# Optimization experiments

Measured on AMD Instinct MI355X. Metric: run time of the kernel, lower is better.

Reference implementation:

```python
import jax, jax.numpy as jnp
import numpy as np

NUM_CAT = 16
SEG_LENS = np.array([4, 2, 2, 4, 4, 3, 3, 2, 4, 6, 2, 6, 3, 3, 3, 3], dtype=np.int64)
SHIFTS = np.concatenate([[0], np.cumsum(SEG_LENS)[:-1]]).astype(np.int64)
MAX_SEG_COUNT = int(SEG_LENS.max())           # 6
MAX_SEG = int(SHIFTS[-1] + SEG_LENS[-1] - 1)  # 53
IN = 128
N = 65536
EPS = 1e-5  # BatchNorm1d default eps
SLOPE = 0.2  # LeakyReLU negative slope


def setup_inputs() -> dict:
    key = jax.random.key(0)
    ks = jax.random.split(key, 4)
    features = jax.random.normal(ks[0], (N, IN), dtype=jnp.float32)
    category_labels = jax.random.randint(ks[1], (N,), 0, NUM_CAT, dtype=jnp.int64)
    # channel raising MLP: Linear(IN -> NUM_CAT*IN, bias=False)
    W1 = jax.random.normal(ks[2], (IN, NUM_CAT * IN), dtype=jnp.float32) * (1.0 / np.sqrt(IN))
    gamma = jnp.ones((NUM_CAT * IN,), dtype=jnp.float32)
    beta = jnp.zeros((NUM_CAT * IN,), dtype=jnp.float32)
    # UnaryConv weight: xavier_normal over (NUM_CAT, IN, MAX_SEG_COUNT)
    W2 = jax.random.normal(ks[3], (NUM_CAT, IN, MAX_SEG_COUNT), dtype=jnp.float32) * np.sqrt(2.0 / (IN + MAX_SEG_COUNT))
    bias = jnp.zeros((MAX_SEG_COUNT,), dtype=jnp.float32)
    return dict(features=features, W1=W1, gamma=gamma, beta=beta, W2=W2, bias=bias,
                category_labels=category_labels)


def reference(features, W1, gamma, beta, W2, bias, category_labels):
    n = features.shape[0]
    # channel raising: Linear -> BatchNorm1d (batch stats) -> LeakyReLU(0.2)
    h = features @ W1                                   # [N, C*D]
    mean = h.mean(axis=0)
    var = h.var(axis=0)                                 # biased, as in torch BN
    h = (h - mean) / jnp.sqrt(var + EPS) * gamma + beta
    h = jnp.where(h >= 0, h, SLOPE * h)
    # per-category batched matmul classifier
    h = h.reshape(n, NUM_CAT, IN).transpose(1, 0, 2)    # [C, N, D]
    logits_all = jnp.einsum('cnd,cds->cns', h, W2) + bias  # [C, N, S]
    n_idx = jnp.arange(n)
    logits = logits_all[category_labels, n_idx]         # gather: [N, S]
    logsm = jax.nn.log_softmax(logits, axis=-1)
    # scatter into per-category segment ranges of the [N, MAX_SEG+1] output
    shifts = jnp.asarray(SHIFTS)[category_labels]       # [N]
    seg_len = jnp.asarray(SEG_LENS)[category_labels]    # [N]
    s_idx = jnp.arange(MAX_SEG_COUNT)
    valid = s_idx[None, :] < seg_len[:, None]           # [N, S]
    cols = jnp.clip(shifts[:, None] + s_idx[None, :], 0, MAX_SEG)
    vals = jnp.where(valid, logsm, 0.0)                 # invalid slots add 0
    out = jnp.zeros((n, MAX_SEG + 1), dtype=logsm.dtype)
    out = out.at[n_idx[:, None], cols].add(vals)
    return out
```

## Files before the change

kernel.cpp:

```cpp
#include <hip/hip_runtime.h>
#include <hip/hip_bf16.h>

#define NCAT 16

typedef __attribute__((ext_vector_type(8))) short short8v;
typedef __attribute__((ext_vector_type(4))) float float4v;
typedef __attribute__((ext_vector_type(16))) float f32x16;

__constant__ int c_shift[NCAT] = {0,4,6,8,12,16,19,22,24,28,34,36,42,45,48,51};
__constant__ int c_len[NCAT]   = {4,2,2,4,4,3,3,2,4,6,2,6,3,3,3,3};


static inline __device__ unsigned pk2(float lo, float hi) {
  float2 f2; f2.x = lo; f2.y = hi;
  __hip_bfloat162 h = __float22bfloat162_rn(f2);
  unsigned u; __builtin_memcpy(&u, &h, 4);
  return u;
}
static inline __device__ float bf2f(unsigned short v) {
  unsigned u = (unsigned)v << 16;
  float f; __builtin_memcpy(&f, &u, 4);
  return f;
}

template<bool PART>
__global__ __launch_bounds__(1024) void k_stats_m(
    const float* __restrict__ F, const float* __restrict__ W1,
    const float* __restrict__ W2,
    float* __restrict__ Gdst, unsigned* __restrict__ Gp16,
    float* __restrict__ sv, float* __restrict__ svpart,
    unsigned short* __restrict__ Wlb, float* __restrict__ W2p)
{
  const int tid = threadIdx.x;
  if (blockIdx.x >= 256) {
    const int cat = (int)blockIdx.x - 256;
    for (int e = tid; e < 2048; e += 1024) {
      const int fid = e >> 6, l = e & 63;
      const int ks = fid >> 3, ct = fid & 7;
      const int kb = 32 * ks + 8 * (l >> 4);
      const int c = cat * 128 + 16 * ct + (l & 15);
      uint4 pk;
      pk.x = pk2(W1[(size_t)(kb + 0) * 2048 + c], W1[(size_t)(kb + 1) * 2048 + c]);
      pk.y = pk2(W1[(size_t)(kb + 2) * 2048 + c], W1[(size_t)(kb + 3) * 2048 + c]);
      pk.z = pk2(W1[(size_t)(kb + 4) * 2048 + c], W1[(size_t)(kb + 5) * 2048 + c]);
      pk.w = pk2(W1[(size_t)(kb + 6) * 2048 + c], W1[(size_t)(kb + 7) * 2048 + c]);
      *(uint4*)(Wlb + ((size_t)(cat * 32 + fid) * 64 + l) * 8) = pk;
    }
    if (tid < 1024) {
      const int c = tid >> 3, s = tid & 7;
      W2p[cat * 1024 + tid] = (s < 6) ? W2[cat * 768 + c * 6 + s] : 0.f;
    }
    return;
  }

  const int rowbase = blockIdx.x * 256;
  const int wid = tid >> 6, lane = tid & 63;
  const int wi = wid >> 2, wj = wid & 3;
  const int i0 = wi * 32, j0 = wj * 32;
  const int lr = lane & 31, lh = lane >> 5;

  f32x16 acc;
  #pragma unroll
  for (int e = 0; e < 16; ++e) acc[e] = 0.f;
  float svacc = 0.f;

  for (int ch = 0; ch < 8; ++ch) {
    #pragma unroll
    for (int h = 0; h < 2; ++h) {
      const int rbase = rowbase + ch * 32 + 16 * h + 8 * lh;
      float fa[8], fb[8];
      #pragma unroll
      for (int j = 0; j < 8; ++j) {
        const float* rp = F + (size_t)(rbase + j) * 128;
        fa[j] = rp[i0 + lr];
        fb[j] = rp[j0 + lr];
      }
      if (wj == 0) {
        #pragma unroll
        for (int j = 0; j < 8; ++j) svacc += fa[j];
      }
      uint4 av4, bv4;
      av4.x = pk2(fa[0], fa[1]); av4.y = pk2(fa[2], fa[3]);
      av4.z = pk2(fa[4], fa[5]); av4.w = pk2(fa[6], fa[7]);
      bv4.x = pk2(fb[0], fb[1]); bv4.y = pk2(fb[2], fb[3]);
      bv4.z = pk2(fb[4], fb[5]); bv4.w = pk2(fb[6], fb[7]);
      acc = __builtin_amdgcn_mfma_f32_32x32x16_bf16(
          __builtin_bit_cast(short8v, av4), __builtin_bit_cast(short8v, bv4),
          acc, 0, 0, 0);
    }
  }

  if (wj == 0) {
    svacc += __shfl_xor(svacc, 32);
    if (lane < 32) {
      if (PART) svpart[blockIdx.x * 128 + i0 + lr] = svacc;
      else      atomicAdd(&sv[i0 + lr], svacc);
    }
  }

  if (PART) {
    unsigned* gp = Gp16 + (size_t)blockIdx.x * 8192;
    #pragma unroll
    for (int t = 0; t < 8; ++t) {
      const int rowe = ((2 * t) & 3) + 8 * (t >> 1) + 4 * lh;
      gp[((i0 + rowe) >> 1) * 128 + j0 + lr] = pk2(acc[2 * t], acc[2 * t + 1]);
    }
  } else {
    #pragma unroll
    for (int reg = 0; reg < 16; ++reg) {
      const int row = (reg & 3) + 8 * (reg >> 2) + 4 * lh;
      atomicAdd(&Gdst[(i0 + row) * 128 + j0 + lr], acc[reg]);
    }
  }
}

__global__ __launch_bounds__(256) void k_reduce(
    const unsigned* __restrict__ Gp16, const float* __restrict__ svpart,
    float* __restrict__ G, float* __restrict__ sv)
{
  const int b = blockIdx.x, tid = threadIdx.x;
  if (b < 64) {
    const int e = b * 128 + (tid >> 1);
    const int half = tid & 1;
    float lo = 0.f, hi = 0.f;
    #pragma unroll 4
    for (int p = half * 128; p < half * 128 + 128; ++p) {
      const unsigned u = Gp16[(size_t)p * 8192 + e];
      lo += bf2f((unsigned short)(u & 0xffffu));
      hi += bf2f((unsigned short)(u >> 16));
    }
    lo += __shfl_xor(lo, 1);
    hi += __shfl_xor(hi, 1);
    if (half == 0) {
      const int pr = e >> 7, col = e & 127;
      G[(2 * pr) * 128 + col]     = lo;
      G[(2 * pr + 1) * 128 + col] = hi;
    }
  } else {
    if (tid < 128) {
      float s = 0.f;
      #pragma unroll 8
      for (int p = 0; p < 256; ++p) s += svpart[p * 128 + tid];
      sv[tid] = s;
    }
  }
}

__global__ __launch_bounds__(256) void k_params(
    const float* __restrict__ G, const float* __restrict__ sv,
    const float* __restrict__ W1, const float* __restrict__ gamma,
    const float* __restrict__ beta, float* __restrict__ scale,
    float* __restrict__ shiftv)
{
  __shared__ float Gl[128][133];
  __shared__ float Wl[128][16];
  __shared__ float redq[16][16];
  __shared__ float redm[16][16];
  const int tid = threadIdx.x;
  const int jb = blockIdx.x * 16;
  for (int i = tid; i < 16384; i += 256) Gl[i >> 7][i & 127] = G[i];
  for (int i = tid; i < 2048; i += 256) {
    int k = i >> 4, col = i & 15;
    Wl[k][col] = W1[(size_t)k * 2048 + jb + col];
  }
  __syncthreads();
  const int col = tid & 15, part = tid >> 4;
  float msq = 0.f, mean = 0.f;
  for (int ii = 0; ii < 8; ++ii) {
    const int i = part * 8 + ii;
    const float wi = Wl[i][col];
    float inner = 0.f;
    #pragma unroll 8
    for (int k = 0; k < 128; ++k) inner = fmaf(Gl[i][k], Wl[k][col], inner);
    msq = fmaf(wi, inner, msq);
  }
  #pragma unroll
  for (int kk = 0; kk < 8; ++kk) {
    const int k = part * 8 + kk;
    mean = fmaf(sv[k], Wl[k][col], mean);
  }
  redq[part][col] = msq;
  redm[part][col] = mean;
  __syncthreads();
  if (tid < 16) {
    float q = 0.f, m = 0.f;
    #pragma unroll
    for (int p = 0; p < 16; ++p) { q += redq[p][tid]; m += redm[p][tid]; }
    m *= (1.f / 65536.f);
    q *= (1.f / 65536.f);
    float var = q - m * m;
    float sc = gamma[jb + tid] * rsqrtf(var + 1e-5f);
    scale[jb + tid] = sc;
    shiftv[jb + tid] = beta[jb + tid] - m * sc;
  }
}

__global__ __launch_bounds__(512, 2) void k_main(
    const float* __restrict__ F, const unsigned short* __restrict__ Wlb,
    const float* __restrict__ W2p, const float* __restrict__ bias,
    const float* __restrict__ scale, const float* __restrict__ shiftv,
    const int* __restrict__ lab, float* __restrict__ out)
{
  __shared__ __attribute__((aligned(16))) float obuf[128 * 54];
  __shared__ unsigned short lrows[128];
  __shared__ int wcs[2][NCAT];
  __shared__ int loff[NCAT + 1];
  __shared__ unsigned char gcat[32], gsub[32];
  __shared__ int gtot;

  const int tid = threadIdx.x;
  const int blk = (int)blockIdx.x;
  const int wid = tid >> 6, lane = tid & 63;
  const int lrow = lane & 15, lhi = lane >> 4;

  {
    float4* ob4 = (float4*)obuf;
    for (int i = tid; i < 1728; i += 512) ob4[i] = make_float4(0.f, 0.f, 0.f, 0.f);
  }

  int myc = 0, myrank = 0;
  if (tid < 128) {
    myc = lab[blk * 128 + tid];
    const unsigned long long lanebit = 1ull << lane;
    #pragma unroll
    for (int cc = 0; cc < NCAT; ++cc) {
      unsigned long long m = __ballot(myc == cc);
      if (lane == 0) wcs[wid][cc] = (int)__popcll(m);
      if (myc == cc) myrank = (int)__popcll(m & (lanebit - 1));
    }
  }
  __syncthreads();
  if (tid == 0) {
    int a = 0, g = 0;
    for (int c = 0; c < NCAT; ++c) {
      loff[c] = a;
      const int cnt = wcs[0][c] + wcs[1][c];
      for (int s2 = 0; s2 * 16 < cnt; ++s2) {
        gcat[g] = (unsigned char)c; gsub[g] = (unsigned char)s2; ++g;
      }
      a += cnt;
    }
    loff[NCAT] = a;
    gtot = g;
  }
  __syncthreads();
  if (tid < 128) {
    const int wbase = (wid == 1) ? wcs[0][myc] : 0;
    lrows[loff[myc] + wbase + myrank] = (unsigned short)tid;
  }
  __syncthreads();

  float bi[6];
  #pragma unroll
  for (int s = 0; s < 6; ++s) bi[s] = bias[s];

  const int ng = gtot;
  int g = wid;
  if (g >= ng) { __syncthreads(); goto dump; }

  {
    float4 cA[4], cB[4];
    {
      const int cat0 = gcat[g];
      const int slot0 = loff[cat0] + ((int)gsub[g] << 4);
      const int hi2 = loff[cat0 + 1];
      const int srow = lrows[min(slot0 + lrow, hi2 - 1)];
      const float* fp = F + ((size_t)(blk * 128 + srow)) * 128 + lhi * 8;
      #pragma unroll
      for (int ks = 0; ks < 4; ++ks) {
        cA[ks] = *(const float4*)(fp + ks * 32);
        cB[ks] = *(const float4*)(fp + ks * 32 + 4);
      }
    }

    for (; g < ng; g += 8) {
      const int cat = gcat[g];
      const int slot0 = loff[cat] + ((int)gsub[g] << 4);
      const int hi2 = loff[cat + 1];
      const int navail = min(16, hi2 - slot0);
      const unsigned short* wbase2 = Wlb + (size_t)cat * 16384;

      const int gn = g + 8;
      const bool hn = gn < ng;
      float4 nA[4], nB[4];
      if (hn) {
        const int catn = gcat[gn];
        const int slot0n = loff[catn] + ((int)gsub[gn] << 4);
        const int hi2n = loff[catn + 1];
        const int srown = lrows[min(slot0n + lrow, hi2n - 1)];
        const float* fpn = F + ((size_t)(blk * 128 + srown)) * 128 + lhi * 8;
        #pragma unroll
        for (int ks = 0; ks < 4; ++ks) {
          nA[ks] = *(const float4*)(fpn + ks * 32);
          nB[ks] = *(const float4*)(fpn + ks * 32 + 4);
        }
      }

      float4v acc[8];
      #pragma unroll
      for (int ct = 0; ct < 8; ++ct) acc[ct] = (float4v){0.f, 0.f, 0.f, 0.f};

      #pragma unroll
      for (int ks = 0; ks < 4; ++ks) {
        uint4 av4;
        av4.x = pk2(cA[ks].x, cA[ks].y); av4.y = pk2(cA[ks].z, cA[ks].w);
        av4.z = pk2(cB[ks].x, cB[ks].y); av4.w = pk2(cB[ks].z, cB[ks].w);
        const short8v av = __builtin_bit_cast(short8v, av4);
        #pragma unroll
        for (int ct = 0; ct < 8; ++ct) {
          short8v bv = *(const short8v*)(wbase2 + ((ks * 8 + ct) * 64 + lane) * 8);
          acc[ct] = __builtin_amdgcn_mfma_f32_16x16x32_bf16(av, bv, acc[ct], 0, 0, 0);
        }
      }

      float p[4][6];
      #pragma unroll
      for (int j = 0; j < 4; ++j)
        #pragma unroll
        for (int s = 0; s < 6; ++s) p[j][s] = 0.f;
      #pragma unroll
      for (int ct = 0; ct < 8; ++ct) {
        const int c = ct * 16 + lrow;
        const float s_ = scale[cat * 128 + c];
        const float h_ = shiftv[cat * 128 + c];
        const float4* w2p4 = (const float4*)(W2p + ((size_t)cat * 128 + c) * 8);
        const float4 wa = w2p4[0];
        const float4 wb = w2p4[1];
        const float w2v[6] = {wa.x, wa.y, wa.z, wa.w, wb.x, wb.y};
        #pragma unroll
        for (int j = 0; j < 4; ++j) {
          float a = acc[ct][j] * s_ + h_;
          a = (a >= 0.f) ? a : 0.2f * a;
          #pragma unroll
          for (int s = 0; s < 6; ++s) p[j][s] = fmaf(a, w2v[s], p[j][s]);
        }
      }
      const bool b1 = (lrow & 1) != 0;
      const bool b2 = (lrow & 2) != 0;
      float q[2][6], r[6];
      #pragma unroll
      for (int t = 0; t < 2; ++t)
        #pragma unroll
        for (int s = 0; s < 6; ++s) {
          float snd = b1 ? p[2 * t][s] : p[2 * t + 1][s];
          float kp  = b1 ? p[2 * t + 1][s] : p[2 * t][s];
          q[t][s] = kp + __shfl_xor(snd, 1);
        }
      #pragma unroll
      for (int s = 0; s < 6; ++s) {
        float snd = b2 ? q[0][s] : q[1][s];
        float kp  = b2 ? q[1][s] : q[0][s];
        r[s] = kp + __shfl_xor(snd, 2);
      }
      #pragma unroll
      for (int s = 0; s < 6; ++s) r[s] += __shfl_xor(r[s], 4);
      #pragma unroll
      for (int s = 0; s < 6; ++s) r[s] += __shfl_xor(r[s], 8);

      const int jj = lrow & 3, sb = lrow >> 2;
      const int jrow = 4 * lhi + jj;
      float pj[6];
      #pragma unroll
      for (int s = 0; s < 6; ++s) pj[s] = r[s] + bi[s];
      float mx = fmaxf(fmaxf(fmaxf(pj[0], pj[1]), fmaxf(pj[2], pj[3])), fmaxf(pj[4], pj[5]));
      float e = __expf(pj[0] - mx) + __expf(pj[1] - mx) + __expf(pj[2] - mx)
              + __expf(pj[3] - mx) + __expf(pj[4] - mx) + __expf(pj[5] - mx);
      float lse = mx + __logf(e);

      if (jrow < navail) {
        const int orow = (int)lrows[slot0 + jrow];
        const int shc = c_shift[cat], lnc = c_len[cat];
        float* ob = obuf + orow * 54 + shc;
        if (sb == 0) {
          ob[0] = pj[0] - lse;
          ob[1] = pj[1] - lse;
          if (lnc > 2) ob[2] = pj[2] - lse;
          if (lnc > 3) ob[3] = pj[3] - lse;
        } else if (sb == 1) {
          if (lnc > 4) ob[4] = pj[4] - lse;
          if (lnc > 5) ob[5] = pj[5] - lse;
        }
      }

      if (hn) {
        #pragma unroll
        for (int ks = 0; ks < 4; ++ks) { cA[ks] = nA[ks]; cB[ks] = nB[ks]; }
      }
    }
    __syncthreads();
  }

dump:
  {
    const float4* ob4 = (const float4*)obuf;
    float4* o4 = (float4*)(out + (size_t)blk * 6912);
    for (int i = tid; i < 1728; i += 512) o4[i] = ob4[i];
  }
}

extern "C" void kernel_launch(void* const* d_in, const int* in_sizes, int n_in,
                              void* d_out, int out_size, void* d_ws, size_t ws_size,
                              hipStream_t stream) {
  const float* F     = (const float*)d_in[0];
  const float* W1    = (const float*)d_in[1];
  const float* gamma = (const float*)d_in[2];
  const float* beta  = (const float*)d_in[3];
  const float* W2    = (const float*)d_in[4];
  const float* bias  = (const float*)d_in[5];
  const int*   lab   = (const int*)d_in[6];
  float* out = (float*)d_out;

  char* ws = (char*)d_ws;
  float* scale   = (float*)(ws + 0);
  float* shiftv  = (float*)(ws + 8192);
  float* G       = (float*)(ws + 16384);
  float* sv      = (float*)(ws + 81920);
  unsigned short* Wlb = (unsigned short*)(ws + 82432);
  float* W2p     = (float*)(ws + 606720);
  unsigned* Gp16 = (unsigned*)(ws + 672256);
  float* svpart  = (float*)(ws + 9060864);

  const size_t need = 9191936;
  if (ws_size >= need) {
    hipLaunchKernelGGL(k_stats_m<true>, dim3(272), dim3(1024), 0, stream,
                       F, W1, W2, G, Gp16, sv, svpart, Wlb, W2p);
    hipLaunchKernelGGL(k_reduce, dim3(65), dim3(256), 0, stream,
                       Gp16, svpart, G, sv);
  } else {
    hipMemsetAsync(ws + 16384, 0, 66048, stream);
    hipLaunchKernelGGL(k_stats_m<false>, dim3(272), dim3(1024), 0, stream,
                       F, W1, W2, G, Gp16, sv, svpart, Wlb, W2p);
  }
  hipLaunchKernelGGL(k_params, dim3(128), dim3(256), 0, stream,
                     G, sv, W1, gamma, beta, scale, shiftv);
  hipLaunchKernelGGL(k_main, dim3(512), dim3(512), 0, stream,
                     F, Wlb, W2p, bias, scale, shiftv, lab, out);
}
```

Measured before the change: 79.71 us.

## Stage block feature tile as swizzled bf16 in LDS instead of per-group gathers

The block's 128x128 fp32 feature tile is now loaded once with coalesced reads, converted to bf16, and stored in LDS with an XOR swizzle. Each wave then reads its A fragments for a category group from LDS, which replaces the gathered global row loads and the software prefetch of the next group. Each row is converted to bf16 once instead of once per group that covers it. This adds 32KB of LDS per block, which may limit occupancy at 2 blocks of 512 threads, and it serialises the feature load ahead of the compute loop instead of overlapping the two.

```diff
diff --git a/kernel.cpp b/kernel.cpp
--- a/kernel.cpp
+++ b/kernel.cpp
@@ -201,6 +201,7 @@
     const float* __restrict__ scale, const float* __restrict__ shiftv,
     const int* __restrict__ lab, float* __restrict__ out)
 {
+  __shared__ __attribute__((aligned(16))) unsigned short Fl[128 * 128];
   __shared__ __attribute__((aligned(16))) float obuf[128 * 54];
   __shared__ unsigned short lrows[128];
   __shared__ int wcs[2][NCAT];
@@ -214,6 +215,17 @@
   const int lrow = lane & 15, lhi = lane >> 4;
 
   {
+    for (int i = tid; i < 2048; i += 512) {
+      const int r = i >> 4, cb = i & 15;
+      const float4* src = (const float4*)(F + ((size_t)(blk * 128 + r)) * 128 + cb * 8);
+      const float4 a0 = src[0];
+      const float4 a1 = src[1];
+      uint4 pk;
+      pk.x = pk2(a0.x, a0.y); pk.y = pk2(a0.z, a0.w);
+      pk.z = pk2(a1.x, a1.y); pk.w = pk2(a1.z, a1.w);
+      const int co = (cb * 16) ^ ((r & 7) << 4);
+      *(uint4*)((char*)Fl + r * 256 + co) = pk;
+    }
     float4* ob4 = (float4*)obuf;
     for (int i = tid; i < 1728; i += 512) ob4[i] = make_float4(0.f, 0.f, 0.f, 0.f);
   }
@@ -255,142 +267,100 @@
   for (int s = 0; s < 6; ++s) bi[s] = bias[s];
 
   const int ng = gtot;
-  int g = wid;
-  if (g >= ng) { __syncthreads(); goto dump; }
-
-  {
-    float4 cA[4], cB[4];
-    {
-      const int cat0 = gcat[g];
-      const int slot0 = loff[cat0] + ((int)gsub[g] << 4);
-      const int hi2 = loff[cat0 + 1];
-      const int srow = lrows[min(slot0 + lrow, hi2 - 1)];
-      const float* fp = F + ((size_t)(blk * 128 + srow)) * 128 + lhi * 8;
-      #pragma unroll
-      for (int ks = 0; ks < 4; ++ks) {
-        cA[ks] = *(const float4*)(fp + ks * 32);
-        cB[ks] = *(const float4*)(fp + ks * 32 + 4);
-      }
-    }
-
-    for (; g < ng; g += 8) {
-      const int cat = gcat[g];
-      const int slot0 = loff[cat] + ((int)gsub[g] << 4);
-      const int hi2 = loff[cat + 1];
-      const int navail = min(16, hi2 - slot0);
-      const unsigned short* wbase2 = Wlb + (size_t)cat * 16384;
-
-      const int gn = g + 8;
-      const bool hn = gn < ng;
-      float4 nA[4], nB[4];
-      if (hn) {
-        const int catn = gcat[gn];
-        const int slot0n = loff[catn] + ((int)gsub[gn] << 4);
-        const int hi2n = loff[catn + 1];
-        const int srown = lrows[min(slot0n + lrow, hi2n - 1)];
-        const float* fpn = F + ((size_t)(blk * 128 + srown)) * 128 + lhi * 8;
-        #pragma unroll
-        for (int ks = 0; ks < 4; ++ks) {
-          nA[ks] = *(const float4*)(fpn + ks * 32);
-          nB[ks] = *(const float4*)(fpn + ks * 32 + 4);
-        }
-      }
-
-      float4v acc[8];
-      #pragma unroll
-      for (int ct = 0; ct < 8; ++ct) acc[ct] = (float4v){0.f, 0.f, 0.f, 0.f};
-
-      #pragma unroll
-      for (int ks = 0; ks < 4; ++ks) {
-        uint4 av4;
-        av4.x = pk2(cA[ks].x, cA[ks].y); av4.y = pk2(cA[ks].z, cA[ks].w);
-        av4.z = pk2(cB[ks].x, cB[ks].y); av4.w = pk2(cB[ks].z, cB[ks].w);
-        const short8v av = __builtin_bit_cast(short8v, av4);
-        #pragma unroll
-        for (int ct = 0; ct < 8; ++ct) {
-          short8v bv = *(const short8v*)(wbase2 + ((ks * 8 + ct) * 64 + lane) * 8);
-          acc[ct] = __builtin_amdgcn_mfma_f32_16x16x32_bf16(av, bv, acc[ct], 0, 0, 0);
-        }
-      }
-
-      float p[4][6];
-      #pragma unroll
-      for (int j = 0; j < 4; ++j)
-        #pragma unroll
-        for (int s = 0; s < 6; ++s) p[j][s] = 0.f;
+  for (int g = wid; g < ng; g += 8) {
+    const int cat = gcat[g];
+    const int slot0 = loff[cat] + ((int)gsub[g] << 4);
+    const int hi2 = loff[cat + 1];
+    const int navail = min(16, hi2 - slot0);
+    const int srow = lrows[min(slot0 + lrow, hi2 - 1)];
+    const unsigned short* wbase2 = Wlb + (size_t)cat * 16384;
+
+    float4v acc[8];
+    #pragma unroll
+    for (int ct = 0; ct < 8; ++ct) acc[ct] = (float4v){0.f, 0.f, 0.f, 0.f};
+
+    #pragma unroll
+    for (int ks = 0; ks < 4; ++ks) {
+      const int co = (ks * 64 + lhi * 16) ^ ((srow & 7) << 4);
+      const short8v av = *(const short8v*)((const char*)Fl + srow * 256 + co);
       #pragma unroll
       for (int ct = 0; ct < 8; ++ct) {
-        const int c = ct * 16 + lrow;
-        const float s_ = scale[cat * 128 + c];
-        const float h_ = shiftv[cat * 128 + c];
-        const float4* w2p4 = (const float4*)(W2p + ((size_t)cat * 128 + c) * 8);
-        const float4 wa = w2p4[0];
-        const float4 wb = w2p4[1];
-        const float w2v[6] = {wa.x, wa.y, wa.z, wa.w, wb.x, wb.y};
+        short8v bv = *(const short8v*)(wbase2 + ((ks * 8 + ct) * 64 + lane) * 8);
+        acc[ct] = __builtin_amdgcn_mfma_f32_16x16x32_bf16(av, bv, acc[ct], 0, 0, 0);
+      }
+    }
+
+    float p[4][6];
+    #pragma unroll
+    for (int j = 0; j < 4; ++j)
+      #pragma unroll
+      for (int s = 0; s < 6; ++s) p[j][s] = 0.f;
+    #pragma unroll
+    for (int ct = 0; ct < 8; ++ct) {
+      const int c = ct * 16 + lrow;
+      const float s_ = scale[cat * 128 + c];
+      const float h_ = shiftv[cat * 128 + c];
+      const float4* w2p4 = (const float4*)(W2p + ((size_t)cat * 128 + c) * 8);
+      const float4 wa = w2p4[0];
+      const float4 wb = w2p4[1];
+      const float w2v[6] = {wa.x, wa.y, wa.z, wa.w, wb.x, wb.y};
+      #pragma unroll
+      for (int j = 0; j < 4; ++j) {
+        float a = acc[ct][j] * s_ + h_;
+        a = (a >= 0.f) ? a : 0.2f * a;
         #pragma unroll
-        for (int j = 0; j < 4; ++j) {
-          float a = acc[ct][j] * s_ + h_;
-          a = (a >= 0.f) ? a : 0.2f * a;
-          #pragma unroll
-          for (int s = 0; s < 6; ++s) p[j][s] = fmaf(a, w2v[s], p[j][s]);
-        }
-      }
-      const bool b1 = (lrow & 1) != 0;
-      const bool b2 = (lrow & 2) != 0;
-      float q[2][6], r[6];
-      #pragma unroll
-      for (int t = 0; t < 2; ++t)
-        #pragma unroll
-        for (int s = 0; s < 6; ++s) {
-          float snd = b1 ? p[2 * t][s] : p[2 * t + 1][s];
-          float kp  = b1 ? p[2 * t + 1][s] : p[2 * t][s];
-          q[t][s] = kp + __shfl_xor(snd, 1);
-        }
+        for (int s = 0; s < 6; ++s) p[j][s] = fmaf(a, w2v[s], p[j][s]);
+      }
+    }
+    const bool b1 = (lrow & 1) != 0;
+    const bool b2 = (lrow & 2) != 0;
+    float q[2][6], r[6];
+    #pragma unroll
+    for (int t = 0; t < 2; ++t)
       #pragma unroll
       for (int s = 0; s < 6; ++s) {
-        float snd = b2 ? q[0][s] : q[1][s];
-        float kp  = b2 ? q[1][s] : q[0][s];
-        r[s] = kp + __shfl_xor(snd, 2);
-      }
-      #pragma unroll
-      for (int s = 0; s < 6; ++s) r[s] += __shfl_xor(r[s], 4);
-      #pragma unroll
-      for (int s = 0; s < 6; ++s) r[s] += __shfl_xor(r[s], 8);
-
-      const int jj = lrow & 3, sb = lrow >> 2;
-      const int jrow = 4 * lhi + jj;
-      float pj[6];
-      #pragma unroll
-      for (int s = 0; s < 6; ++s) pj[s] = r[s] + bi[s];
-      float mx = fmaxf(fmaxf(fmaxf(pj[0], pj[1]), fmaxf(pj[2], pj[3])), fmaxf(pj[4], pj[5]));
-      float e = __expf(pj[0] - mx) + __expf(pj[1] - mx) + __expf(pj[2] - mx)
-              + __expf(pj[3] - mx) + __expf(pj[4] - mx) + __expf(pj[5] - mx);
-      float lse = mx + __logf(e);
-
-      if (jrow < navail) {
-        const int orow = (int)lrows[slot0 + jrow];
-        const int shc = c_shift[cat], lnc = c_len[cat];
-        float* ob = obuf + orow * 54 + shc;
-        if (sb == 0) {
-          ob[0] = pj[0] - lse;
-          ob[1] = pj[1] - lse;
-          if (lnc > 2) ob[2] = pj[2] - lse;
-          if (lnc > 3) ob[3] = pj[3] - lse;
-        } else if (sb == 1) {
-          if (lnc > 4) ob[4] = pj[4] - lse;
-          if (lnc > 5) ob[5] = pj[5] - lse;
-        }
-      }
-
-      if (hn) {
-        #pragma unroll
-        for (int ks = 0; ks < 4; ++ks) { cA[ks] = nA[ks]; cB[ks] = nB[ks]; }
-      }
-    }
-    __syncthreads();
-  }
-
-dump:
+        float snd = b1 ? p[2 * t][s] : p[2 * t + 1][s];
+        float kp  = b1 ? p[2 * t + 1][s] : p[2 * t][s];
+        q[t][s] = kp + __shfl_xor(snd, 1);
+      }
+    #pragma unroll
+    for (int s = 0; s < 6; ++s) {
+      float snd = b2 ? q[0][s] : q[1][s];
+      float kp  = b2 ? q[1][s] : q[0][s];
+      r[s] = kp + __shfl_xor(snd, 2);
+    }
+    #pragma unroll
+    for (int s = 0; s < 6; ++s) r[s] += __shfl_xor(r[s], 4);
+    #pragma unroll
+    for (int s = 0; s < 6; ++s) r[s] += __shfl_xor(r[s], 8);
+
+    const int jj = lrow & 3, sb = lrow >> 2;
+    const int jrow = 4 * lhi + jj;
+    float pj[6];
+    #pragma unroll
+    for (int s = 0; s < 6; ++s) pj[s] = r[s] + bi[s];
+    float mx = fmaxf(fmaxf(fmaxf(pj[0], pj[1]), fmaxf(pj[2], pj[3])), fmaxf(pj[4], pj[5]));
+    float e = __expf(pj[0] - mx) + __expf(pj[1] - mx) + __expf(pj[2] - mx)
+            + __expf(pj[3] - mx) + __expf(pj[4] - mx) + __expf(pj[5] - mx);
+    float lse = mx + __logf(e);
+
+    if (jrow < navail) {
+      const int orow = (int)lrows[slot0 + jrow];
+      const int shc = c_shift[cat], lnc = c_len[cat];
+      float* ob = obuf + orow * 54 + shc;
+      if (sb == 0) {
+        ob[0] = pj[0] - lse;
+        ob[1] = pj[1] - lse;
+        if (lnc > 2) ob[2] = pj[2] - lse;
+        if (lnc > 3) ob[3] = pj[3] - lse;
+      } else if (sb == 1) {
+        if (lnc > 4) ob[4] = pj[4] - lse;
+        if (lnc > 5) ob[5] = pj[5] - lse;
+      }
+    }
+  }
+  __syncthreads();
+
   {
     const float4* ob4 = (const float4*)obuf;
     float4* o4 = (float4*)(out + (size_t)blk * 6912);
```

Result: no change. 78.45 us (-1.6%).
